# Performance work log

Measured on AMD Instinct MI355X. Metric: run time of the kernel, lower is better.

The kernel has to match this reference:

```python
import jax, jax.numpy as jnp
import numpy as np
import math

B, T, D, H = 4, 2048, 1024, 16
HD = D // H  # 64

def setup_inputs() -> dict:
    key = jax.random.key(0)
    ks = jax.random.split(key, 11)
    s = 1.0 / math.sqrt(D)
    return {
        "q": jax.random.normal(ks[0], (B, T, D), jnp.float32),
        "k": jax.random.normal(ks[1], (B, T, D), jnp.float32),
        "v": jax.random.normal(ks[2], (B, T, D), jnp.float32),
        "Wq": jax.random.normal(ks[3], (D, D), jnp.float32) * s,
        "bq": jnp.zeros((D,), jnp.float32),
        "Wk": jax.random.normal(ks[4], (D, D), jnp.float32) * s,
        "bk": jnp.zeros((D,), jnp.float32),
        "Wv": jax.random.normal(ks[5], (D, D), jnp.float32) * s,
        "bv": jnp.zeros((D,), jnp.float32),
        "Wo": jax.random.normal(ks[6], (D, D), jnp.float32) * s,
        "bo": jnp.zeros((D,), jnp.float32),
    }

def reference(q, k, v, Wq, bq, Wk, bk, Wv, bv, Wo, bo):
    # Linear projections (torch Linear: x @ W.T + b)
    qp = q @ Wq.T + bq
    kp = k @ Wk.T + bk
    vp = v @ Wv.T + bv
    # [B, T, D] -> [B, H, T, HD]
    def split(x):
        return x.reshape(B, T, H, HD).transpose(0, 2, 1, 3)
    qh, kh, vh = split(qp), split(kp), split(vp)
    # scaled dot-product attention
    score = jnp.einsum('bhqd,bhkd->bhqk', qh, kh) / math.sqrt(HD)
    attn = jax.nn.softmax(score, axis=-1)
    out = jnp.einsum('bhqk,bhkd->bhqd', attn, vh)
    # merge heads and output projection
    out = out.transpose(0, 2, 1, 3).reshape(B, T, D)
    return out @ Wo.T + bo
```

## Files before the change

kernel.cpp:

```cpp
#include <hip/hip_runtime.h>
#include <hip/hip_bf16.h>
#include <stdint.h>

#define B_ 4
#define T_ 2048
#define D_ 1024
#define H_ 16
#define HD_ 64
#define NKT (T_ / 64)

typedef __bf16 bf16;
typedef __bf16 bf16x8 __attribute__((ext_vector_type(8)));
typedef __bf16 bf16x4 __attribute__((ext_vector_type(4)));
typedef float f32x4 __attribute__((ext_vector_type(4)));

#define QSCALE 0.18033688011112042f

__device__ __forceinline__ float fast_exp2(float x) {
#if __has_builtin(__builtin_amdgcn_exp2f)
    return __builtin_amdgcn_exp2f(x);
#else
    return exp2f(x);
#endif
}

__device__ __forceinline__ void async_load16(const bf16* g, const bf16* lds_uniform) {
    __builtin_amdgcn_global_load_lds(
        (const __attribute__((address_space(1))) uint32_t*)(uintptr_t)g,
        (__attribute__((address_space(3))) uint32_t*)(uintptr_t)lds_uniform,
        16, 0, 0);
}

__global__ __launch_bounds__(256) void cast3(const float* __restrict__ s0, bf16* __restrict__ d0,
                                             const float* __restrict__ s1, bf16* __restrict__ d1,
                                             const float* __restrict__ s2, bf16* __restrict__ d2,
                                             int n4) {
    const float* s = blockIdx.y == 0 ? s0 : (blockIdx.y == 1 ? s1 : s2);
    bf16* d = blockIdx.y == 0 ? d0 : (blockIdx.y == 1 ? d1 : d2);
    int i = blockIdx.x * 256 + threadIdx.x;
    if (i < n4) {
        f32x4 v = ((const f32x4*)s)[i];
        bf16x4 o;
        o.x = (bf16)v.x; o.y = (bf16)v.y; o.z = (bf16)v.z; o.w = (bf16)v.w;
        ((bf16x4*)d)[i] = o;
    }
}

__global__ __launch_bounds__(256) void cast4(const float* __restrict__ s0, bf16* __restrict__ d0,
                                             const float* __restrict__ s1, bf16* __restrict__ d1,
                                             const float* __restrict__ s2, bf16* __restrict__ d2,
                                             const float* __restrict__ s3, bf16* __restrict__ d3,
                                             int n4) {
    const float* s = blockIdx.y == 0 ? s0 : (blockIdx.y == 1 ? s1 : (blockIdx.y == 2 ? s2 : s3));
    bf16* d = blockIdx.y == 0 ? d0 : (blockIdx.y == 1 ? d1 : (blockIdx.y == 2 ? d2 : d3));
    int i = blockIdx.x * 256 + threadIdx.x;
    if (i < n4) {
        f32x4 v = ((const f32x4*)s)[i];
        bf16x4 o;
        o.x = (bf16)v.x; o.y = (bf16)v.y; o.z = (bf16)v.z; o.w = (bf16)v.w;
        ((bf16x4*)d)[i] = o;
    }
}

template <typename OutT, int VMODE>
__global__ __launch_bounds__(256) void gemm_nt(const bf16* __restrict__ A,
                                               const bf16* __restrict__ W,
                                               const float* __restrict__ bias,
                                               OutT* __restrict__ C,
                                               int M, int N, int K, float scale) {
    __shared__ bf16 As[2][128 * 32];
    __shared__ bf16 Bs[2][128 * 32];
    const int tid = threadIdx.x;
    const int wid = tid >> 6, lane = tid & 63;
    const int quad = lane >> 4, l15 = lane & 15;
    const int wm = (wid >> 1) * 64, wn = (wid & 1) * 64;
    const int bx = N >> 7;
    const int lin = blockIdx.x;
    const int ty = (lin & 7) + 8 * (lin / (8 * bx));
    const int tx = (lin >> 3) % bx;
    const long rowA0 = (long)ty * 128;
    const long rowB0 = (long)tx * 128;
    const int srow = lane >> 2;
    const int schunk = (lane & 3) * 8;
    const int sbase = (wid * 32) * 32;

    f32x4 acc[4][4];
#pragma unroll
    for (int i = 0; i < 4; i++)
#pragma unroll
        for (int j = 0; j < 4; j++) acc[i][j] = (f32x4){0.f, 0.f, 0.f, 0.f};

#pragma unroll
    for (int s = 0; s < 2; s++) {
        int r = wid * 32 + s * 16 + srow;
        async_load16(&A[(rowA0 + r) * K + schunk], &As[0][sbase + s * 16 * 32]);
        async_load16(&W[(rowB0 + r) * K + schunk], &Bs[0][sbase + s * 16 * 32]);
    }
    __syncthreads();

    const int NIT = K >> 5;
    for (int it = 0; it < NIT; it++) {
        const int cur = it & 1;
        if (it + 1 < NIT) {
            const int k1 = (it + 1) << 5, nb = cur ^ 1;
#pragma unroll
            for (int s = 0; s < 2; s++) {
                int r = wid * 32 + s * 16 + srow;
                async_load16(&A[(rowA0 + r) * K + k1 + schunk], &As[nb][sbase + s * 16 * 32]);
                async_load16(&W[(rowB0 + r) * K + k1 + schunk], &Bs[nb][sbase + s * 16 * 32]);
            }
        }
        bf16x8 af[4], bfr[4];
#pragma unroll
        for (int i = 0; i < 4; i++)
            af[i] = *(const bf16x8*)&As[cur][(wm + i * 16 + l15) * 32 + quad * 8];
#pragma unroll
        for (int j = 0; j < 4; j++)
            bfr[j] = *(const bf16x8*)&Bs[cur][(wn + j * 16 + l15) * 32 + quad * 8];
#pragma unroll
        for (int i = 0; i < 4; i++)
#pragma unroll
            for (int j = 0; j < 4; j++)
                acc[i][j] = __builtin_amdgcn_mfma_f32_16x16x32_bf16(af[i], bfr[j],
                                                                    acc[i][j], 0, 0, 0);
        __syncthreads();
    }

    if constexpr (VMODE == 0) {
#pragma unroll
        for (int i = 0; i < 4; i++) {
            long m = rowA0 + wm + i * 16 + quad * 4;
#pragma unroll
            for (int j = 0; j < 4; j++) {
                long n = rowB0 + wn + j * 16 + l15;
                float bb = bias[n];
#pragma unroll
                for (int r = 0; r < 4; r++) {
                    float v = (acc[i][j][r] + bb) * scale;
                    C[(m + r) * N + n] = (OutT)v;
                }
            }
        }
    } else {
        __shared__ bf16 Tt[128 * 136];
#pragma unroll
        for (int i = 0; i < 4; i++) {
            int ml = wm + i * 16 + quad * 4;
#pragma unroll
            for (int j = 0; j < 4; j++) {
                int nl = wn + j * 16 + l15;
                float bb = bias[rowB0 + nl];
                bf16x4 ov = {(bf16)(acc[i][j][0] + bb), (bf16)(acc[i][j][1] + bb),
                             (bf16)(acc[i][j][2] + bb), (bf16)(acc[i][j][3] + bb)};
                *(bf16x4*)&Tt[nl * 136 + ml] = ov;
            }
        }
        __syncthreads();
        const long bidx = rowA0 >> 11;
        const int t0 = (int)(rowA0 & 2047);
#pragma unroll
        for (int p = 0; p < 8; p++) {
            int nl = p * 16 + (tid >> 4);
            int c = tid & 15;
            bf16x8 val = *(const bf16x8*)&Tt[nl * 136 + c * 8];
            int n = (int)rowB0 + nl;
            long vrow = (bidx * H_ + (n >> 6)) * (long)HD_ + (n & 63);
            *(bf16x8*)&((bf16*)C)[vrow * T_ + t0 + c * 8] = val;
        }
    }
}

__global__ __launch_bounds__(256) void attn_kernel(const bf16* __restrict__ Qp,
                                                   const bf16* __restrict__ Kp,
                                                   const bf16* __restrict__ VT,
                                                   bf16* __restrict__ Op) {
    __shared__ bf16 Ks[2][64 * 64];
    __shared__ bf16 Vs[2][64 * 64];
    __shared__ bf16 Ps[4 * 64 * 64];
    const int tid = threadIdx.x;
    const int wid = tid >> 6, lane = tid & 63;
    const int quad = lane >> 4, l15 = lane & 15;
    const int q7 = l15 & 7;
    const int lin = blockIdx.x;
    const int bh = (lin & 7) + 8 * (lin >> 6);
    const int qt = (lin >> 3) & 7;
    const int b = bh >> 4, h = bh & 15;
    const long tok0 = (long)b * T_ + (long)qt * 256 + wid * 64;
    const int hcol = h * HD_;
    const long vrow0 = ((long)bh) * HD_;
    bf16* Ps_w = &Ps[wid * 64 * 64];
    const int g_sw = ((lane & 7) ^ (lane >> 3)) * 8;
    const int srow = lane >> 3;
    const int sbase = (wid * 16) * 64;

    {
        const long krow0 = (long)b * T_;
#pragma unroll
        for (int s = 0; s < 2; s++) {
            int r = wid * 16 + s * 8 + srow;
            async_load16(&Kp[(krow0 + r) * D_ + hcol + g_sw], &Ks[0][sbase + s * 8 * 64]);
            async_load16(&VT[(vrow0 + r) * T_ + g_sw], &Vs[0][sbase + s * 8 * 64]);
        }
    }

    bf16x8 bq[4][2];
#pragma unroll
    for (int nt = 0; nt < 4; nt++)
#pragma unroll
        for (int ks = 0; ks < 2; ks++)
            bq[nt][ks] = *(const bf16x8*)&Qp[(tok0 + nt * 16 + l15) * D_ + hcol +
                                             ks * 32 + quad * 8];

    f32x4 o[4][4];
#pragma unroll
    for (int mt = 0; mt < 4; mt++)
#pragma unroll
        for (int nt = 0; nt < 4; nt++) o[mt][nt] = (f32x4){0.f, 0.f, 0.f, 0.f};
    float lsum[4] = {0.f, 0.f, 0.f, 0.f};

    __syncthreads();

    for (int kt = 0; kt < NKT; kt++) {
        const int cur = kt & 1;
        if (kt + 1 < NKT) {
            const long krow1 = (long)b * T_ + (long)(kt + 1) * 64;
            const int nb = cur ^ 1;
#pragma unroll
            for (int s = 0; s < 2; s++) {
                int r = wid * 16 + s * 8 + srow;
                async_load16(&Kp[(krow1 + r) * D_ + hcol + g_sw], &Ks[nb][sbase + s * 8 * 64]);
                async_load16(&VT[(vrow0 + r) * T_ + (long)(kt + 1) * 64 + g_sw],
                             &Vs[nb][sbase + s * 8 * 64]);
            }
        }

        bf16x8 pb0[4], pb1[4];
#pragma unroll
        for (int mt = 0; mt < 2; mt++) {
            bf16x8 ak0 = *(const bf16x8*)&Ks[cur][(mt * 16 + l15) * 64 + ((quad ^ q7) * 8)];
            bf16x8 ak1 = *(const bf16x8*)&Ks[cur][(mt * 16 + l15) * 64 + (((4 + quad) ^ q7) * 8)];
#pragma unroll
            for (int nt = 0; nt < 4; nt++) {
                f32x4 s = {0.f, 0.f, 0.f, 0.f};
                s = __builtin_amdgcn_mfma_f32_16x16x32_bf16(ak0, bq[nt][0], s, 0, 0, 0);
                s = __builtin_amdgcn_mfma_f32_16x16x32_bf16(ak1, bq[nt][1], s, 0, 0, 0);
                float p0 = fast_exp2(s[0]), p1 = fast_exp2(s[1]);
                float p2 = fast_exp2(s[2]), p3 = fast_exp2(s[3]);
                lsum[nt] += (p0 + p1) + (p2 + p3);
                bf16x4 pv = {(bf16)p0, (bf16)p1, (bf16)p2, (bf16)p3};
                *(bf16x4*)&Ps_w[(nt * 16 + l15) * 64 +
                                (((mt * 2 + (quad >> 1)) ^ q7) * 8) + (quad & 1) * 4] = pv;
            }
        }
#pragma unroll
        for (int nt = 0; nt < 4; nt++)
            pb0[nt] = *(const bf16x8*)&Ps_w[(nt * 16 + l15) * 64 + ((quad ^ q7) * 8)];
#pragma unroll
        for (int mt = 2; mt < 4; mt++) {
            bf16x8 ak0 = *(const bf16x8*)&Ks[cur][(mt * 16 + l15) * 64 + ((quad ^ q7) * 8)];
            bf16x8 ak1 = *(const bf16x8*)&Ks[cur][(mt * 16 + l15) * 64 + (((4 + quad) ^ q7) * 8)];
#pragma unroll
            for (int nt = 0; nt < 4; nt++) {
                f32x4 s = {0.f, 0.f, 0.f, 0.f};
                s = __builtin_amdgcn_mfma_f32_16x16x32_bf16(ak0, bq[nt][0], s, 0, 0, 0);
                s = __builtin_amdgcn_mfma_f32_16x16x32_bf16(ak1, bq[nt][1], s, 0, 0, 0);
                float p0 = fast_exp2(s[0]), p1 = fast_exp2(s[1]);
                float p2 = fast_exp2(s[2]), p3 = fast_exp2(s[3]);
                lsum[nt] += (p0 + p1) + (p2 + p3);
                bf16x4 pv = {(bf16)p0, (bf16)p1, (bf16)p2, (bf16)p3};
                *(bf16x4*)&Ps_w[(nt * 16 + l15) * 64 +
                                (((mt * 2 + (quad >> 1)) ^ q7) * 8) + (quad & 1) * 4] = pv;
            }
        }
#pragma unroll
        for (int mt = 0; mt < 4; mt++) {
            bf16x8 av0 = *(const bf16x8*)&Vs[cur][(mt * 16 + l15) * 64 + ((quad ^ q7) * 8)];
#pragma unroll
            for (int nt = 0; nt < 4; nt++)
                o[mt][nt] = __builtin_amdgcn_mfma_f32_16x16x32_bf16(av0, pb0[nt],
                                                                    o[mt][nt], 0, 0, 0);
        }
#pragma unroll
        for (int nt = 0; nt < 4; nt++)
            pb1[nt] = *(const bf16x8*)&Ps_w[(nt * 16 + l15) * 64 + (((4 + quad) ^ q7) * 8)];
#pragma unroll
        for (int mt = 0; mt < 4; mt++) {
            bf16x8 av1 = *(const bf16x8*)&Vs[cur][(mt * 16 + l15) * 64 + (((4 + quad) ^ q7) * 8)];
#pragma unroll
            for (int nt = 0; nt < 4; nt++)
                o[mt][nt] = __builtin_amdgcn_mfma_f32_16x16x32_bf16(av1, pb1[nt],
                                                                    o[mt][nt], 0, 0, 0);
        }
        __syncthreads();
    }

#pragma unroll
    for (int nt = 0; nt < 4; nt++) {
        lsum[nt] += __shfl_xor(lsum[nt], 16, 64);
        lsum[nt] += __shfl_xor(lsum[nt], 32, 64);
        lsum[nt] = 1.f / lsum[nt];
    }

#pragma unroll
    for (int mt = 0; mt < 4; mt++)
#pragma unroll
        for (int nt = 0; nt < 4; nt++) {
            bf16x4 ov = {(bf16)(o[mt][nt][0] * lsum[nt]), (bf16)(o[mt][nt][1] * lsum[nt]),
                         (bf16)(o[mt][nt][2] * lsum[nt]), (bf16)(o[mt][nt][3] * lsum[nt])};
            *(bf16x4*)&Ps_w[(nt * 16 + l15) * 64 +
                            (((mt * 2 + (quad >> 1)) ^ q7) * 8) + (quad & 1) * 4] = ov;
        }
#pragma unroll
    for (int p2 = 0; p2 < 8; p2++) {
        int q = p2 * 8 + (lane >> 3);
        int dc = lane & 7;
        bf16x8 ov = *(const bf16x8*)&Ps_w[q * 64 + ((dc ^ (q & 7)) * 8)];
        *(bf16x8*)&Op[(tok0 + q) * D_ + hcol + dc * 8] = ov;
    }
}

extern "C" void kernel_launch(void* const* d_in, const int* in_sizes, int n_in,
                              void* d_out, int out_size, void* d_ws, size_t ws_size,
                              hipStream_t stream) {
    const float* q  = (const float*)d_in[0];
    const float* k  = (const float*)d_in[1];
    const float* v  = (const float*)d_in[2];
    const float* Wq = (const float*)d_in[3];
    const float* bq = (const float*)d_in[4];
    const float* Wk = (const float*)d_in[5];
    const float* bk = (const float*)d_in[6];
    const float* Wv = (const float*)d_in[7];
    const float* bv = (const float*)d_in[8];
    const float* Wo = (const float*)d_in[9];
    const float* bo = (const float*)d_in[10];
    float* out = (float*)d_out;

    const size_t MD = (size_t)B_ * T_ * D_;
    const size_t DD = (size_t)D_ * D_;
    char* ws = (char*)d_ws;
    bf16* Xq  = (bf16*)ws; ws += MD * 2;
    bf16* Xk  = (bf16*)ws; ws += MD * 2;
    bf16* Xv  = (bf16*)ws; ws += MD * 2;
    bf16* WqB = (bf16*)ws; ws += DD * 2;
    bf16* WkB = (bf16*)ws; ws += DD * 2;
    bf16* WvB = (bf16*)ws; ws += DD * 2;
    bf16* WoB = (bf16*)ws; ws += DD * 2;
    bf16* Qp  = (bf16*)ws; ws += MD * 2;
    bf16* Kp  = (bf16*)ws; ws += MD * 2;
    bf16* VtG = (bf16*)ws; ws += MD * 2;
    bf16* Op  = (bf16*)ws; ws += MD * 2;

    cast3<<<dim3(MD / 4 / 256, 3), 256, 0, stream>>>(q, Xq, k, Xk, v, Xv, MD / 4);
    cast4<<<dim3(DD / 4 / 256, 4), 256, 0, stream>>>(Wq, WqB, Wk, WkB, Wv, WvB, Wo, WoB, DD / 4);

    const int nblk = (B_ * T_ / 128) * (D_ / 128);
    gemm_nt<bf16, 0><<<nblk, 256, 0, stream>>>(Xq, WqB, bq, Qp, B_ * T_, D_, D_, QSCALE);
    gemm_nt<bf16, 0><<<nblk, 256, 0, stream>>>(Xk, WkB, bk, Kp, B_ * T_, D_, D_, 1.f);
    gemm_nt<bf16, 1><<<nblk, 256, 0, stream>>>(Xv, WvB, bv, VtG, B_ * T_, D_, D_, 1.f);

    attn_kernel<<<B_ * H_ * (T_ / 256), 256, 0, stream>>>(Qp, Kp, VtG, Op);

    gemm_nt<float, 0><<<nblk, 256, 0, stream>>>(Op, WoB, bo, out, B_ * T_, D_, D_, 1.f);
}
```

Measured before the change: 340.6 us.

## Keep softmax probabilities in registers via permlane16 swap instead of LDS round-trip

The attention kernel no longer writes the exponentiated scores to a per-wave LDS buffer and reads them back as MFMA B operands. It packs them into bf16 pairs and uses v_permlane16_swap to rearrange them in registers. To make that in-register layout match, the V-transpose projection epilogue now permutes 8-element chunks within each group of 32 tokens when storing V^T. Shared memory shrinks from 64KB to 32KB, with the K/V buffers reused as epilogue staging, which may allow more resident blocks. The cost is extra VALU permute work and a V layout that is tied to this specific fragment mapping.

```diff
diff --git a/kernel.cpp b/kernel.cpp
--- a/kernel.cpp
+++ b/kernel.cpp
@@ -13,6 +13,7 @@
 typedef __bf16 bf16x8 __attribute__((ext_vector_type(8)));
 typedef __bf16 bf16x4 __attribute__((ext_vector_type(4)));
 typedef float f32x4 __attribute__((ext_vector_type(4)));
+typedef uint32_t u32x4 __attribute__((ext_vector_type(4)));
 
 #define QSCALE 0.18033688011112042f
 
@@ -29,6 +30,17 @@
         (const __attribute__((address_space(1))) uint32_t*)(uintptr_t)g,
         (__attribute__((address_space(3))) uint32_t*)(uintptr_t)lds_uniform,
         16, 0, 0);
+}
+
+__device__ __forceinline__ uint32_t pack2_bf16(float lo, float hi) {
+    union { uint32_t u; __bf16 h[2]; } r;
+    r.h[0] = (__bf16)lo;
+    r.h[1] = (__bf16)hi;
+    return r.u;
+}
+
+__device__ __forceinline__ void permswap16(uint32_t& a, uint32_t& b) {
+    asm("v_permlane16_swap_b32 %0, %1" : "+v"(a), "+v"(b));
 }
 
 __global__ __launch_bounds__(256) void cast3(const float* __restrict__ s0, bf16* __restrict__ d0,
@@ -165,7 +177,8 @@
             bf16x8 val = *(const bf16x8*)&Tt[nl * 136 + c * 8];
             int n = (int)rowB0 + nl;
             long vrow = (bidx * H_ + (n >> 6)) * (long)HD_ + (n & 63);
-            *(bf16x8*)&((bf16*)C)[vrow * T_ + t0 + c * 8] = val;
+            int cp = (c & ~3) | ((c & 1) << 1) | ((c & 2) >> 1);
+            *(bf16x8*)&((bf16*)C)[vrow * T_ + t0 + cp * 8] = val;
         }
     }
 }
@@ -174,9 +187,7 @@
                                                    const bf16* __restrict__ Kp,
                                                    const bf16* __restrict__ VT,
                                                    bf16* __restrict__ Op) {
-    __shared__ bf16 Ks[2][64 * 64];
-    __shared__ bf16 Vs[2][64 * 64];
-    __shared__ bf16 Ps[4 * 64 * 64];
+    __shared__ bf16 smem[4][64 * 64];
     const int tid = threadIdx.x;
     const int wid = tid >> 6, lane = tid & 63;
     const int quad = lane >> 4, l15 = lane & 15;
@@ -188,7 +199,6 @@
     const long tok0 = (long)b * T_ + (long)qt * 256 + wid * 64;
     const int hcol = h * HD_;
     const long vrow0 = ((long)bh) * HD_;
-    bf16* Ps_w = &Ps[wid * 64 * 64];
     const int g_sw = ((lane & 7) ^ (lane >> 3)) * 8;
     const int srow = lane >> 3;
     const int sbase = (wid * 16) * 64;
@@ -198,8 +208,8 @@
 #pragma unroll
         for (int s = 0; s < 2; s++) {
             int r = wid * 16 + s * 8 + srow;
-            async_load16(&Kp[(krow0 + r) * D_ + hcol + g_sw], &Ks[0][sbase + s * 8 * 64]);
-            async_load16(&VT[(vrow0 + r) * T_ + g_sw], &Vs[0][sbase + s * 8 * 64]);
+            async_load16(&Kp[(krow0 + r) * D_ + hcol + g_sw], &smem[0][sbase + s * 8 * 64]);
+            async_load16(&VT[(vrow0 + r) * T_ + g_sw], &smem[2][sbase + s * 8 * 64]);
         }
     }
 
@@ -228,64 +238,80 @@
 #pragma unroll
             for (int s = 0; s < 2; s++) {
                 int r = wid * 16 + s * 8 + srow;
-                async_load16(&Kp[(krow1 + r) * D_ + hcol + g_sw], &Ks[nb][sbase + s * 8 * 64]);
+                async_load16(&Kp[(krow1 + r) * D_ + hcol + g_sw], &smem[nb][sbase + s * 8 * 64]);
                 async_load16(&VT[(vrow0 + r) * T_ + (long)(kt + 1) * 64 + g_sw],
-                             &Vs[nb][sbase + s * 8 * 64]);
-            }
-        }
-
-        bf16x8 pb0[4], pb1[4];
-#pragma unroll
-        for (int mt = 0; mt < 2; mt++) {
-            bf16x8 ak0 = *(const bf16x8*)&Ks[cur][(mt * 16 + l15) * 64 + ((quad ^ q7) * 8)];
-            bf16x8 ak1 = *(const bf16x8*)&Ks[cur][(mt * 16 + l15) * 64 + (((4 + quad) ^ q7) * 8)];
+                             &smem[2 + nb][sbase + s * 8 * 64]);
+            }
+        }
+        const bf16* Ksc = smem[cur];
+        const bf16* Vsc = smem[2 + cur];
+
+        bf16x8 pb0[4];
+        {
+            uint32_t pA[2][4], pB[2][4];
+#pragma unroll
+            for (int mt = 0; mt < 2; mt++) {
+                bf16x8 ak0 = *(const bf16x8*)&Ksc[(mt * 16 + l15) * 64 + ((quad ^ q7) * 8)];
+                bf16x8 ak1 = *(const bf16x8*)&Ksc[(mt * 16 + l15) * 64 + (((4 + quad) ^ q7) * 8)];
+#pragma unroll
+                for (int nt = 0; nt < 4; nt++) {
+                    f32x4 s = {0.f, 0.f, 0.f, 0.f};
+                    s = __builtin_amdgcn_mfma_f32_16x16x32_bf16(ak0, bq[nt][0], s, 0, 0, 0);
+                    s = __builtin_amdgcn_mfma_f32_16x16x32_bf16(ak1, bq[nt][1], s, 0, 0, 0);
+                    float p0 = fast_exp2(s[0]), p1 = fast_exp2(s[1]);
+                    float p2 = fast_exp2(s[2]), p3 = fast_exp2(s[3]);
+                    lsum[nt] += (p0 + p1) + (p2 + p3);
+                    pA[mt][nt] = pack2_bf16(p0, p1);
+                    pB[mt][nt] = pack2_bf16(p2, p3);
+                }
+            }
 #pragma unroll
             for (int nt = 0; nt < 4; nt++) {
-                f32x4 s = {0.f, 0.f, 0.f, 0.f};
-                s = __builtin_amdgcn_mfma_f32_16x16x32_bf16(ak0, bq[nt][0], s, 0, 0, 0);
-                s = __builtin_amdgcn_mfma_f32_16x16x32_bf16(ak1, bq[nt][1], s, 0, 0, 0);
-                float p0 = fast_exp2(s[0]), p1 = fast_exp2(s[1]);
-                float p2 = fast_exp2(s[2]), p3 = fast_exp2(s[3]);
-                lsum[nt] += (p0 + p1) + (p2 + p3);
-                bf16x4 pv = {(bf16)p0, (bf16)p1, (bf16)p2, (bf16)p3};
-                *(bf16x4*)&Ps_w[(nt * 16 + l15) * 64 +
-                                (((mt * 2 + (quad >> 1)) ^ q7) * 8) + (quad & 1) * 4] = pv;
-            }
-        }
-#pragma unroll
-        for (int nt = 0; nt < 4; nt++)
-            pb0[nt] = *(const bf16x8*)&Ps_w[(nt * 16 + l15) * 64 + ((quad ^ q7) * 8)];
-#pragma unroll
-        for (int mt = 2; mt < 4; mt++) {
-            bf16x8 ak0 = *(const bf16x8*)&Ks[cur][(mt * 16 + l15) * 64 + ((quad ^ q7) * 8)];
-            bf16x8 ak1 = *(const bf16x8*)&Ks[cur][(mt * 16 + l15) * 64 + (((4 + quad) ^ q7) * 8)];
-#pragma unroll
-            for (int nt = 0; nt < 4; nt++) {
-                f32x4 s = {0.f, 0.f, 0.f, 0.f};
-                s = __builtin_amdgcn_mfma_f32_16x16x32_bf16(ak0, bq[nt][0], s, 0, 0, 0);
-                s = __builtin_amdgcn_mfma_f32_16x16x32_bf16(ak1, bq[nt][1], s, 0, 0, 0);
-                float p0 = fast_exp2(s[0]), p1 = fast_exp2(s[1]);
-                float p2 = fast_exp2(s[2]), p3 = fast_exp2(s[3]);
-                lsum[nt] += (p0 + p1) + (p2 + p3);
-                bf16x4 pv = {(bf16)p0, (bf16)p1, (bf16)p2, (bf16)p3};
-                *(bf16x4*)&Ps_w[(nt * 16 + l15) * 64 +
-                                (((mt * 2 + (quad >> 1)) ^ q7) * 8) + (quad & 1) * 4] = pv;
+                permswap16(pA[0][nt], pA[1][nt]);
+                permswap16(pB[0][nt], pB[1][nt]);
+                u32x4 f = {pA[0][nt], pB[0][nt], pA[1][nt], pB[1][nt]};
+                pb0[nt] = __builtin_bit_cast(bf16x8, f);
             }
         }
 #pragma unroll
         for (int mt = 0; mt < 4; mt++) {
-            bf16x8 av0 = *(const bf16x8*)&Vs[cur][(mt * 16 + l15) * 64 + ((quad ^ q7) * 8)];
+            bf16x8 av0 = *(const bf16x8*)&Vsc[(mt * 16 + l15) * 64 + ((quad ^ q7) * 8)];
 #pragma unroll
             for (int nt = 0; nt < 4; nt++)
                 o[mt][nt] = __builtin_amdgcn_mfma_f32_16x16x32_bf16(av0, pb0[nt],
                                                                     o[mt][nt], 0, 0, 0);
         }
-#pragma unroll
-        for (int nt = 0; nt < 4; nt++)
-            pb1[nt] = *(const bf16x8*)&Ps_w[(nt * 16 + l15) * 64 + (((4 + quad) ^ q7) * 8)];
+        bf16x8 pb1[4];
+        {
+            uint32_t pA[2][4], pB[2][4];
+#pragma unroll
+            for (int mt = 0; mt < 2; mt++) {
+                bf16x8 ak0 = *(const bf16x8*)&Ksc[((2 + mt) * 16 + l15) * 64 + ((quad ^ q7) * 8)];
+                bf16x8 ak1 = *(const bf16x8*)&Ksc[((2 + mt) * 16 + l15) * 64 +
+                                                  (((4 + quad) ^ q7) * 8)];
+#pragma unroll
+                for (int nt = 0; nt < 4; nt++) {
+                    f32x4 s = {0.f, 0.f, 0.f, 0.f};
+                    s = __builtin_amdgcn_mfma_f32_16x16x32_bf16(ak0, bq[nt][0], s, 0, 0, 0);
+                    s = __builtin_amdgcn_mfma_f32_16x16x32_bf16(ak1, bq[nt][1], s, 0, 0, 0);
+                    float p0 = fast_exp2(s[0]), p1 = fast_exp2(s[1]);
+                    float p2 = fast_exp2(s[2]), p3 = fast_exp2(s[3]);
+                    lsum[nt] += (p0 + p1) + (p2 + p3);
+                    pA[mt][nt] = pack2_bf16(p0, p1);
+                    pB[mt][nt] = pack2_bf16(p2, p3);
+                }
+            }
+#pragma unroll
+            for (int nt = 0; nt < 4; nt++) {
+                permswap16(pA[0][nt], pA[1][nt]);
+                permswap16(pB[0][nt], pB[1][nt]);
+                u32x4 f = {pA[0][nt], pB[0][nt], pA[1][nt], pB[1][nt]};
+                pb1[nt] = __builtin_bit_cast(bf16x8, f);
+            }
+        }
 #pragma unroll
         for (int mt = 0; mt < 4; mt++) {
-            bf16x8 av1 = *(const bf16x8*)&Vs[cur][(mt * 16 + l15) * 64 + (((4 + quad) ^ q7) * 8)];
+            bf16x8 av1 = *(const bf16x8*)&Vsc[(mt * 16 + l15) * 64 + (((4 + quad) ^ q7) * 8)];
 #pragma unroll
             for (int nt = 0; nt < 4; nt++)
                 o[mt][nt] = __builtin_amdgcn_mfma_f32_16x16x32_bf16(av1, pb1[nt],
@@ -301,20 +327,21 @@
         lsum[nt] = 1.f / lsum[nt];
     }
 
+    bf16* ew = &smem[wid][0];
 #pragma unroll
     for (int mt = 0; mt < 4; mt++)
 #pragma unroll
         for (int nt = 0; nt < 4; nt++) {
             bf16x4 ov = {(bf16)(o[mt][nt][0] * lsum[nt]), (bf16)(o[mt][nt][1] * lsum[nt]),
                          (bf16)(o[mt][nt][2] * lsum[nt]), (bf16)(o[mt][nt][3] * lsum[nt])};
-            *(bf16x4*)&Ps_w[(nt * 16 + l15) * 64 +
-                            (((mt * 2 + (quad >> 1)) ^ q7) * 8) + (quad & 1) * 4] = ov;
+            *(bf16x4*)&ew[(nt * 16 + l15) * 64 +
+                          (((mt * 2 + (quad >> 1)) ^ q7) * 8) + (quad & 1) * 4] = ov;
         }
 #pragma unroll
     for (int p2 = 0; p2 < 8; p2++) {
         int q = p2 * 8 + (lane >> 3);
         int dc = lane & 7;
-        bf16x8 ov = *(const bf16x8*)&Ps_w[q * 64 + ((dc ^ (q & 7)) * 8)];
+        bf16x8 ov = *(const bf16x8*)&ew[q * 64 + ((dc ^ (q & 7)) * 8)];
         *(bf16x8*)&Op[(tok0 + q) * D_ + hcol + dc * 8] = ov;
     }
 }
```

Result: no change. 342.8 us (+0.6%).
